# Kernel optimization log

Hardware: AMD Instinct MI355X
Metric: run time of the kernel (lower is better)

## Reference

```python
import jax, jax.numpy as jnp
import numpy as np
import math

B, S, D = 16, 256, 41
LATENT, NREF, NLAYERS, NHEADS = 128, 128, 3, 4


def setup_inputs() -> dict:
    key = jax.random.key(0)
    ks = jax.random.split(key, 12)
    time_x = jax.random.uniform(ks[0], (B, S), dtype=jnp.float32)
    value_x = jax.random.normal(ks[1], (B, S, D), dtype=jnp.float32)
    mask_x = jax.random.randint(ks[2], (B, S, D), 0, 2).astype(jnp.int32)
    s = 0.05
    Wi = jax.random.normal(ks[3], (D + 2, LATENT), dtype=jnp.float32) * s
    bi = jnp.zeros((LATENT,), jnp.float32)
    I = jax.random.normal(ks[4], (NLAYERS, NREF, LATENT), dtype=jnp.float32) * s
    # axis 1: 0 -> mab0 (induced->data), 1 -> mab1 (data->induced)
    Wq = jax.random.normal(ks[5], (NLAYERS, 2, LATENT, LATENT), dtype=jnp.float32) * s
    Wk = jax.random.normal(ks[6], (NLAYERS, 2, LATENT, LATENT), dtype=jnp.float32) * s
    Wv = jax.random.normal(ks[7], (NLAYERS, 2, LATENT, LATENT), dtype=jnp.float32) * s
    Wo = jax.random.normal(ks[8], (NLAYERS, 2, LATENT, LATENT), dtype=jnp.float32) * s
    bq = jnp.zeros((NLAYERS, 2, LATENT), jnp.float32)
    bk = jnp.zeros((NLAYERS, 2, LATENT), jnp.float32)
    bv = jnp.zeros((NLAYERS, 2, LATENT), jnp.float32)
    bo = jnp.zeros((NLAYERS, 2, LATENT), jnp.float32)
    return dict(time_x=time_x, value_x=value_x, mask_x=mask_x, Wi=Wi, bi=bi, I=I,
                Wq=Wq, bq=bq, Wk=Wk, bk=bk, Wv=Wv, bv=bv, Wo=Wo, bo=bo)


def _mab(Q, K, Wq, bq, Wk, bk, Wv, bv, Wo, bo, key_mask):
    # MAB2: multi-head attn (heads via split-last-dim), residual Q_, then O + relu(fc_o(O))
    dV = Wq.shape[1]
    dh = dV // NHEADS
    Bq, Lq, _ = Q.shape
    Qh = (Q @ Wq + bq).reshape(Bq, Lq, NHEADS, dh)
    Kh = (K @ Wk + bk).reshape(Bq, -1, NHEADS, dh)
    Vh = (K @ Wv + bv).reshape(Bq, -1, NHEADS, dh)
    att = jnp.einsum('bqhd,bkhd->bhqk', Qh, Kh) / math.sqrt(dV)
    if key_mask is not None:
        att = jnp.where(key_mask[:, None, None, :] == 0, -10e9, att)
    A = jax.nn.softmax(att, axis=-1)
    O = (Qh + jnp.einsum('bhqk,bkhd->bqhd', A, Vh)).reshape(Bq, Lq, dV)
    return O + jax.nn.relu(O @ Wo + bo)


def reference(time_x, value_x, mask_x, Wi, bi, I, Wq, bq, Wk, bk, Wv, bv, Wo, bo):
    L = S * D
    mflat = mask_x.reshape(B, L)
    # stable compaction: valid entries first, original row-major order preserved
    order = jnp.argsort(1 - mflat, axis=1)  # jnp.argsort is stable
    T = jnp.broadcast_to(time_x[:, :, None], (B, S, D)).reshape(B, L)
    C = jnp.broadcast_to(jnp.arange(D, dtype=jnp.int32), (B, S, D)).reshape(B, L)
    U = value_x.reshape(B, L)
    g = lambda a: jnp.take_along_axis(a, order, axis=1)
    T_, U_, C_, mk_i = g(T), g(U), g(C), g(mflat)
    mk = mk_i.astype(jnp.float32)  # [B, L]
    Coh = jax.nn.one_hot(C_, D, dtype=jnp.float32)
    X = jnp.concatenate([Coh, T_[..., None], U_[..., None]], axis=-1) * mk[..., None]
    Z = jax.nn.relu(X @ Wi + bi) * mk[..., None]  # Y_e, [B, L, LATENT]
    for l in range(NLAYERS):
        Ib = jnp.broadcast_to(I[l][None], (B, NREF, LATENT))
        H = _mab(Ib, Z, Wq[l, 0], bq[l, 0], Wk[l, 0], bk[l, 0], Wv[l, 0], bv[l, 0],
                 Wo[l, 0], bo[l, 0], mk)          # induced points attend to masked data
        O = _mab(Z, H, Wq[l, 1], bq[l, 1], Wk[l, 1], bk[l, 1], Wv[l, 1], bv[l, 1],
                 Wo[l, 1], bo[l, 1], None)        # data attends to induced points (all valid)
        Z = O * mk[..., None] + Z
    return Z, mk[..., None]
```

## Files before the change

### kernel.cpp

```cpp
#include <hip/hip_runtime.h>
#include <math.h>

#define BB 16
#define SS 256
#define DD 41
#define LL (SS*DD)
#define LAT 128
#define NH 4
#define NL 3
#define RSQ 0.08838834764831845f

typedef short bf16x8 __attribute__((ext_vector_type(8)));
typedef float f32x4 __attribute__((ext_vector_type(4)));
#define MFMA __builtin_amdgcn_mfma_f32_16x16x32_bf16

__device__ __forceinline__ unsigned short f2b(float f) {
    unsigned u = __builtin_bit_cast(unsigned, f);
    unsigned r = (u + 0x7FFFu + ((u >> 16) & 1u)) >> 16;
    return (unsigned short)r;
}
__device__ __forceinline__ float b2f(unsigned short h) {
    unsigned u = ((unsigned)h) << 16;
    return __builtin_bit_cast(float, u);
}

__global__ __launch_bounds__(256)
void k_compact(const float* __restrict__ time_x, const float* __restrict__ value_x,
               const int* __restrict__ mask_x,
               float* __restrict__ compT, float* __restrict__ compU,
               int* __restrict__ compC, int* __restrict__ nvalid)
{
    int b = blockIdx.x, tid = threadIdx.x;
    int lane = tid & 63, w = tid >> 6;
    __shared__ int sW[4];
    __shared__ int s_base;
    if (tid == 0) s_base = 0;
    __syncthreads();
    for (int j0 = 0; j0 < LL; j0 += 256) {
        int j = j0 + tid;
        int m = mask_x[b * LL + j];
        unsigned long long bal = __ballot(m != 0);
        int pre = __popcll(bal & ((1ull << lane) - 1ull));
        if (lane == 0) sW[w] = __popcll(bal);
        __syncthreads();
        int woff = 0;
        for (int i = 0; i < w; ++i) woff += sW[i];
        int tot = sW[0] + sW[1] + sW[2] + sW[3];
        if (m) {
            int pos = s_base + woff + pre;
            compT[b * LL + pos] = time_x[b * SS + j / DD];
            compU[b * LL + pos] = value_x[b * LL + j];
            compC[b * LL + pos] = j % DD;
        }
        __syncthreads();
        if (tid == 0) s_base += tot;
        __syncthreads();
    }
    if (tid == 0) nvalid[b] = s_base;
}

template<int UZ>
__global__ __launch_bounds__(256)
void k_init(const float* __restrict__ Wi, const float* __restrict__ bi,
            const float* __restrict__ compT, const float* __restrict__ compU,
            const int* __restrict__ compC, const int* __restrict__ nvalid,
            float* __restrict__ out, unsigned short* __restrict__ Zb)
{
    int b = blockIdx.y, p0 = blockIdx.x * 8, tid = threadIdx.x;
    float* Z = out;
    float* MK = out + (size_t)BB * LL * LAT;
    int nv = nvalid[b];
    for (int s = 0; s < 2; ++s) {
        int e = s * 256 + tid;
        int r = e >> 6, k2 = (e & 63) * 2;
        int p = p0 + r;
        size_t zi = ((size_t)b * LL + p) * LAT + k2;
        float v0 = 0.f, v1 = 0.f;
        if (p < nv) {
            int c = compC[b * LL + p];
            float t = compT[b * LL + p], u = compU[b * LL + p];
            v0 = fmaxf(Wi[c * LAT + k2]     + t * Wi[41 * LAT + k2]     + u * Wi[42 * LAT + k2]     + bi[k2],     0.f);
            v1 = fmaxf(Wi[c * LAT + k2 + 1] + t * Wi[41 * LAT + k2 + 1] + u * Wi[42 * LAT + k2 + 1] + bi[k2 + 1], 0.f);
        }
        *(float2*)&Z[zi] = make_float2(v0, v1);
        if constexpr (UZ) {
            unsigned short h2[2] = {f2b(v0), f2b(v1)};
            *(unsigned*)&Zb[((size_t)b * LL + p) * LAT + k2] = *(const unsigned*)h2;
        }
        if (k2 == 0) MK[b * LL + p] = (p < nv) ? 1.f : 0.f;
    }
}

__global__ __launch_bounds__(256)
void k_prep(const float* __restrict__ I, const float* __restrict__ Wq,
            const float* __restrict__ bq,
            const float* __restrict__ Wk, const float* __restrict__ Wv,
            const float* __restrict__ Wo,
            float* __restrict__ Qh0f, unsigned short* __restrict__ Qh0b,
            unsigned short* __restrict__ WkT, unsigned short* __restrict__ WvT,
            unsigned short* __restrict__ WqT, unsigned short* __restrict__ WoT)
{
    __shared__ float srow[128];
    int blk = blockIdx.x, tid = threadIdx.x, l = blockIdx.y;
    const float* Il  = I  + (size_t)l * 16384;
    const float* Wq0 = Wq + (size_t)(l * 2 + 0) * 16384;
    const float* bq0 = bq + (size_t)(l * 2 + 0) * 128;
    const float* Wk0 = Wk + (size_t)(l * 2 + 0) * 16384;
    const float* Wv0 = Wv + (size_t)(l * 2 + 0) * 16384;
    const float* Wq1 = Wq + (size_t)(l * 2 + 1) * 16384;
    const float* Wo1 = Wo + (size_t)(l * 2 + 1) * 16384;
    if (blk < 128) {
        if (tid < 128) srow[tid] = Il[blk * 128 + tid];
        __syncthreads();
        if (tid < 128) {
            float acc = bq0[tid];
            for (int i = 0; i < 128; ++i) acc += srow[i] * Wq0[i * 128 + tid];
            Qh0f[(size_t)l * 16384 + blk * 128 + tid] = acc;
            Qh0b[(size_t)l * 16384 + blk * 128 + tid] = f2b(acc);
        }
    } else {
        const float* src = (blk == 128) ? Wk0 : (blk == 129) ? Wv0 : (blk == 130) ? Wq1 : Wo1;
        unsigned short* dst = (blk == 128) ? WkT : (blk == 129) ? WvT : (blk == 130) ? WqT : WoT;
        dst += (size_t)l * 16384;
        for (int e = tid; e < 16384; e += 256) {
            int i = e >> 7, n = e & 127;
            dst[n * 128 + i] = f2b(src[e]);
        }
    }
}

template<int UZ>
__global__ __launch_bounds__(512, 4)
void k_flash0(const float* __restrict__ Z, const unsigned short* __restrict__ Zb,
              const unsigned short* __restrict__ Qh0b,
              const unsigned short* __restrict__ WkT, const unsigned short* __restrict__ WvT,
              const float* __restrict__ bk0, const float* __restrict__ bv0,
              const int* __restrict__ nvalid, float* __restrict__ ml,
              unsigned short* __restrict__ accp, int ks)
{
    const int chunk = blockIdx.x, b = blockIdx.y;
    const int tid = threadIdx.x, lane = tid & 63, w = tid >> 6;
    const int l16 = lane & 15, g4 = lane >> 4;
    const f32x4 fz = {0.f, 0.f, 0.f, 0.f};

    __shared__ unsigned short sZ[32 * 136];
    __shared__ unsigned short sKh[32 * 136];
    __shared__ unsigned short sVT[128 * 40];
    __shared__ float sS[128 * 33];
    __shared__ unsigned short sP[128 * 40];
    __shared__ float sM[NH * 128], sL[NH * 128], sScale[128];

    for (int e = tid; e < NH * 128; e += 512) { sM[e] = -1e30f; sL[e] = 0.f; }

    f32x4 acc[8];
    for (int n = 0; n < 8; ++n) acc[n] = fz;

    int nv = nvalid[b];
    int c0 = (int)(((long long)chunk * nv) / ks);
    int c1 = (int)(((long long)(chunk + 1) * nv) / ks);

    float bkd = bk0[w * 16 + l16];
    float bvd = bv0[w * 16 + l16];

    const int sr = tid >> 4, sc = (tid & 15) * 8;
    float4 pa, pb;
    uint4 pz;
    if (c0 < c1) {
        if constexpr (UZ) {
            pz = *(const uint4*)&Zb[((size_t)b * LL + c0 + sr) * LAT + sc];
        } else {
            const float* s = &Z[((size_t)b * LL + c0 + sr) * LAT + sc];
            pa = *(const float4*)s; pb = *(const float4*)(s + 4);
        }
    }

    __syncthreads();

    for (int kt = c0; kt < c1; kt += 32) {
        int nk = min(32, c1 - kt);
        if constexpr (UZ) {
            uint4 z4 = {0u, 0u, 0u, 0u};
            *(uint4*)&sZ[sr * 136 + sc] = (sr < nk) ? pz : z4;
        } else {
            bf16x8 v;
            if (sr < nk) {
                ((unsigned short*)&v)[0] = f2b(pa.x);
                ((unsigned short*)&v)[1] = f2b(pa.y);
                ((unsigned short*)&v)[2] = f2b(pa.z);
                ((unsigned short*)&v)[3] = f2b(pa.w);
                ((unsigned short*)&v)[4] = f2b(pb.x);
                ((unsigned short*)&v)[5] = f2b(pb.y);
                ((unsigned short*)&v)[6] = f2b(pb.z);
                ((unsigned short*)&v)[7] = f2b(pb.w);
            } else {
                #pragma unroll
                for (int j = 0; j < 8; ++j) ((unsigned short*)&v)[j] = 0;
            }
            *(bf16x8*)&sZ[sr * 136 + sc] = v;
        }
        __syncthreads();
        if (kt + 32 < c1) {
            if constexpr (UZ) {
                pz = *(const uint4*)&Zb[((size_t)b * LL + kt + 32 + sr) * LAT + sc];
            } else {
                const float* s = &Z[((size_t)b * LL + kt + 32 + sr) * LAT + sc];
                pa = *(const float4*)s; pb = *(const float4*)(s + 4);
            }
        }
        {
            f32x4 ck[2] = {fz, fz}, cv[2] = {fz, fz};
            #pragma unroll
            for (int k = 0; k < 4; ++k) {
                bf16x8 a0 = *(const bf16x8*)&sZ[(l16) * 136 + k * 32 + g4 * 8];
                bf16x8 a1 = *(const bf16x8*)&sZ[(16 + l16) * 136 + k * 32 + g4 * 8];
                bf16x8 bk_ = *(const bf16x8*)&WkT[(w * 16 + l16) * 128 + k * 32 + g4 * 8];
                bf16x8 bv_ = *(const bf16x8*)&WvT[(w * 16 + l16) * 128 + k * 32 + g4 * 8];
                ck[0] = MFMA(a0, bk_, ck[0], 0, 0, 0);
                ck[1] = MFMA(a1, bk_, ck[1], 0, 0, 0);
                cv[0] = MFMA(a0, bv_, cv[0], 0, 0, 0);
                cv[1] = MFMA(a1, bv_, cv[1], 0, 0, 0);
            }
            #pragma unroll
            for (int m = 0; m < 2; ++m)
                #pragma unroll
                for (int r = 0; r < 4; ++r) {
                    int kk = m * 16 + g4 * 4 + r;
                    int d = w * 16 + l16;
                    sKh[kk * 136 + d] = f2b(ck[m][r] + bkd);
                    sVT[d * 40 + kk] = f2b(cv[m][r] + bvd);
                }
        }
        __syncthreads();
        for (int h = 0; h < NH; ++h) {
            bf16x8 aq = *(const bf16x8*)&Qh0b[(w * 16 + l16) * 128 + h * 32 + g4 * 8];
            #pragma unroll
            for (int n = 0; n < 2; ++n) {
                bf16x8 bk_ = *(const bf16x8*)&sKh[(n * 16 + l16) * 136 + h * 32 + g4 * 8];
                f32x4 s = MFMA(aq, bk_, fz, 0, 0, 0);
                #pragma unroll
                for (int r = 0; r < 4; ++r)
                    sS[(w * 16 + g4 * 4 + r) * 33 + n * 16 + l16] = s[r] * RSQ;
            }
            int q = w * 16 + (lane >> 2);
            int k0 = (lane & 3) * 8;
            float sv[8];
            float mx = -1e30f;
            #pragma unroll
            for (int j = 0; j < 8; ++j) {
                int kk = k0 + j;
                sv[j] = (kk < nk) ? sS[q * 33 + kk] : -1e30f;
                mx = fmaxf(mx, sv[j]);
            }
            mx = fmaxf(mx, __shfl_xor(mx, 1));
            mx = fmaxf(mx, __shfl_xor(mx, 2));
            float mr = sM[h * 128 + q];
            float mn = fmaxf(mr, mx);
            float sc = __expf(mr - mn);
            float ls = 0.f;
            bf16x8 pv;
            #pragma unroll
            for (int j = 0; j < 8; ++j) {
                float p = (k0 + j < nk) ? __expf(sv[j] - mn) : 0.f;
                ((unsigned short*)&pv)[j] = f2b(p);
                ls += p;
            }
            *(bf16x8*)&sP[q * 40 + k0] = pv;
            ls += __shfl_xor(ls, 1);
            ls += __shfl_xor(ls, 2);
            if ((lane & 3) == 0) {
                sM[h * 128 + q] = mn;
                sL[h * 128 + q] = sL[h * 128 + q] * sc + ls;
                sScale[q] = sc;
            }
            #pragma unroll
            for (int nn = 0; nn < 2; ++nn) {
                int nt = 2 * h + nn;
                #pragma unroll
                for (int r = 0; r < 4; ++r) {
                    float scq = sScale[w * 16 + g4 * 4 + r];
                    acc[nt][r] *= scq;
                }
            }
            bf16x8 aP = *(const bf16x8*)&sP[(w * 16 + l16) * 40 + g4 * 8];
            #pragma unroll
            for (int nn = 0; nn < 2; ++nn) {
                bf16x8 bV = *(const bf16x8*)&sVT[(h * 32 + nn * 16 + l16) * 40 + g4 * 8];
                acc[2 * h + nn] = MFMA(aP, bV, acc[2 * h + nn], 0, 0, 0);
            }
        }
        __syncthreads();
    }
    __syncthreads();
    size_t mlbase = (((size_t)b * ks + chunk) * NH) * 128 * 2;
    for (int e = tid; e < NH * 128; e += 512) {
        ml[mlbase + e * 2 + 0] = sM[e];
        ml[mlbase + e * 2 + 1] = sL[e];
    }
    size_t abase = (((size_t)b * ks + chunk) * 128) * 128;
    #pragma unroll
    for (int n = 0; n < 8; ++n)
        #pragma unroll
        for (int r = 0; r < 4; ++r) {
            int q = w * 16 + g4 * 4 + r;
            int d = n * 16 + l16;
            accp[abase + (size_t)q * 128 + d] = f2b(acc[n][r]);
        }
}

__global__ __launch_bounds__(128)
void k_post0(const float* __restrict__ ml, const unsigned short* __restrict__ accp,
             const float* __restrict__ Qh0f,
             const float* __restrict__ Wo0, const float* __restrict__ bo0,
             const float* __restrict__ Wk1, const float* __restrict__ bk1,
             const float* __restrict__ Wv1, const float* __restrict__ bv1,
             unsigned short* __restrict__ Kh1b, unsigned short* __restrict__ Vh1Tb, int ks)
{
    int q = blockIdx.x, b = blockIdx.y, d = threadIdx.x, h = d >> 5;
    __shared__ float sx[128], sh2[128];
    float M = -1e30f;
    for (int c = 0; c < ks; ++c)
        M = fmaxf(M, ml[((((size_t)b * ks + c) * NH + h) * 128 + q) * 2]);
    float L = 0.f, A = 0.f;
    for (int c = 0; c < ks; ++c) {
        size_t base = ((((size_t)b * ks + c) * NH + h) * 128 + q) * 2;
        float sc = __expf(ml[base] - M);
        L += sc * ml[base + 1];
        A += sc * b2f(accp[(((size_t)b * ks + c) * 128 + q) * 128 + d]);
    }
    float o0 = Qh0f[q * 128 + d] + ((L > 0.f) ? A / L : 0.f);
    sx[d] = o0;
    __syncthreads();
    float acc = bo0[d];
    for (int i = 0; i < 128; ++i) acc += sx[i] * Wo0[i * 128 + d];
    float hv = o0 + fmaxf(acc, 0.f);
    sh2[d] = hv;
    __syncthreads();
    float ak = bk1[d], av = bv1[d];
    for (int i = 0; i < 128; ++i) {
        float x = sh2[i];
        ak += x * Wk1[i * 128 + d];
        av += x * Wv1[i * 128 + d];
    }
    Kh1b[((size_t)b * 128 + q) * 128 + d] = f2b(ak);
    Vh1Tb[((size_t)b * 128 + d) * 128 + q] = f2b(av);
}

template<int UZ>
__global__ __launch_bounds__(512, 6)
void k_mab1(float* __restrict__ Z, unsigned short* __restrict__ Zb,
            const unsigned short* __restrict__ Kh1b,
            const unsigned short* __restrict__ Vh1Tb,
            const unsigned short* __restrict__ WqT, const float* __restrict__ bq1,
            const unsigned short* __restrict__ WoT, const float* __restrict__ bo1,
            const int* __restrict__ nvalid, int writeZb)
{
    const int b = blockIdx.y;
    const int p0 = blockIdx.x * 64;
    const int nv = nvalid[b];
    if (p0 >= nv) return;
    const int tid = threadIdx.x, lane = tid & 63, w = tid >> 6;
    const int l16 = lane & 15, g4 = lane >> 4;
    const f32x4 fz = {0.f, 0.f, 0.f, 0.f};

    __shared__ unsigned short sQh[64 * 136];
    __shared__ unsigned short sU[8 * 16 * 136];
    float* sUf = (float*)sU;

    {
        int r = tid >> 3, c = (tid & 7) * 16;
        if constexpr (UZ) {
            const uint4* zsrc = (const uint4*)&Zb[((size_t)b * LL + p0 + r) * LAT + c];
            *(uint4*)&sU[r * 136 + c]     = zsrc[0];
            *(uint4*)&sU[r * 136 + c + 8] = zsrc[1];
        } else {
            const float* zr = &Z[((size_t)b * LL + p0 + r) * LAT + c];
            #pragma unroll
            for (int half = 0; half < 2; ++half) {
                float4 f0 = *(const float4*)(zr + half * 8);
                float4 f1 = *(const float4*)(zr + half * 8 + 4);
                bf16x8 v;
                ((unsigned short*)&v)[0] = f2b(f0.x);
                ((unsigned short*)&v)[1] = f2b(f0.y);
                ((unsigned short*)&v)[2] = f2b(f0.z);
                ((unsigned short*)&v)[3] = f2b(f0.w);
                ((unsigned short*)&v)[4] = f2b(f1.x);
                ((unsigned short*)&v)[5] = f2b(f1.y);
                ((unsigned short*)&v)[6] = f2b(f1.z);
                ((unsigned short*)&v)[7] = f2b(f1.w);
                *(bf16x8*)&sU[r * 136 + c + half * 8] = v;
            }
        }
    }
    __syncthreads();
    {
        f32x4 c4[4] = {fz, fz, fz, fz};
        #pragma unroll
        for (int ks = 0; ks < 4; ++ks) {
            bf16x8 bw = *(const bf16x8*)&WqT[(w * 16 + l16) * 128 + ks * 32 + g4 * 8];
            #pragma unroll
            for (int mt = 0; mt < 4; ++mt) {
                bf16x8 a = *(const bf16x8*)&sU[(mt * 16 + l16) * 136 + ks * 32 + g4 * 8];
                c4[mt] = MFMA(a, bw, c4[mt], 0, 0, 0);
            }
        }
        float bqv = bq1[w * 16 + l16];
        #pragma unroll
        for (int mt = 0; mt < 4; ++mt)
            #pragma unroll
            for (int r = 0; r < 4; ++r)
                sQh[(mt * 16 + g4 * 4 + r) * 136 + w * 16 + l16] = f2b(c4[mt][r] + bqv);
    }
    __syncthreads();

    const int t = w >> 1;
    const int hbase = (w & 1) * 2;
    unsigned short* ps = &sU[w * 16 * 136];
    f32x4 oacc[2][2];

    #pragma unroll
    for (int hh = 0; hh < 2; ++hh) {
        const int h = hbase + hh;
        f32x4 s[8];
        bf16x8 bq8 = *(const bf16x8*)&sQh[(t * 16 + l16) * 136 + h * 32 + g4 * 8];
        #pragma unroll
        for (int mt = 0; mt < 8; ++mt) {
            bf16x8 ak = *(const bf16x8*)&Kh1b[((size_t)b * 128 + mt * 16 + l16) * 128 + h * 32 + g4 * 8];
            s[mt] = MFMA(ak, bq8, fz, 0, 0, 0);
        }
        float mx = -1e30f;
        #pragma unroll
        for (int mt = 0; mt < 8; ++mt)
            #pragma unroll
            for (int r = 0; r < 4; ++r) mx = fmaxf(mx, s[mt][r]);
        mx = fmaxf(mx, __shfl_xor(mx, 16));
        mx = fmaxf(mx, __shfl_xor(mx, 32));
        float ls = 0.f;
        #pragma unroll
        for (int mt = 0; mt < 8; ++mt)
            #pragma unroll
            for (int r = 0; r < 4; ++r) {
                float p = __expf((s[mt][r] - mx) * RSQ);
                s[mt][r] = p;
                ls += p;
            }
        ls += __shfl_xor(ls, 16);
        ls += __shfl_xor(ls, 32);
        float inv = 1.f / ls;
        #pragma unroll
        for (int mt = 0; mt < 8; ++mt) {
            unsigned short p4[4];
            #pragma unroll
            for (int r = 0; r < 4; ++r) p4[r] = f2b(s[mt][r] * inv);
            *(uint2*)&ps[l16 * 136 + mt * 16 + g4 * 4] = *(const uint2*)p4;
        }
        #pragma unroll
        for (int nn = 0; nn < 2; ++nn) {
            f32x4 o = fz;
            #pragma unroll
            for (int ks = 0; ks < 4; ++ks) {
                bf16x8 aP = *(const bf16x8*)&ps[l16 * 136 + ks * 32 + g4 * 8];
                bf16x8 bV = *(const bf16x8*)&Vh1Tb[((size_t)b * 128 + h * 32 + nn * 16 + l16) * 128 + ks * 32 + g4 * 8];
                o = MFMA(aP, bV, o, 0, 0, 0);
            }
            oacc[hh][nn] = o;
        }
    }
    #pragma unroll
    for (int hh = 0; hh < 2; ++hh)
        #pragma unroll
        for (int nn = 0; nn < 2; ++nn) {
            int col = (hbase + hh) * 32 + nn * 16 + l16;
            #pragma unroll
            for (int r = 0; r < 4; ++r) {
                int row = t * 16 + g4 * 4 + r;
                float val = oacc[hh][nn][r] + b2f(sQh[row * 136 + col]);
                sQh[row * 136 + col] = f2b(val);
            }
        }
    __syncthreads();
    {
        f32x4 c4[4] = {fz, fz, fz, fz};
        #pragma unroll
        for (int ks = 0; ks < 4; ++ks) {
            bf16x8 bw = *(const bf16x8*)&WoT[(w * 16 + l16) * 128 + ks * 32 + g4 * 8];
            #pragma unroll
            for (int mt = 0; mt < 4; ++mt) {
                bf16x8 a = *(const bf16x8*)&sQh[(mt * 16 + l16) * 136 + ks * 32 + g4 * 8];
                c4[mt] = MFMA(a, bw, c4[mt], 0, 0, 0);
            }
        }
        float bov = bo1[w * 16 + l16];
        #pragma unroll
        for (int mt = 0; mt < 4; ++mt)
            #pragma unroll
            for (int r = 0; r < 4; ++r) {
                int row = mt * 16 + g4 * 4 + r;
                sUf[row * 132 + w * 16 + l16] = fmaxf(c4[mt][r] + bov, 0.f);
            }
    }
    __syncthreads();
    {
        int row = tid >> 3, cc = (tid & 7) * 16;
        if (p0 + row < nv) {
            size_t zi = ((size_t)b * LL + p0 + row) * LAT + cc;
            float vout[16];
            const unsigned short* ob = &sQh[row * 136 + cc];
            const float* rf = &sUf[row * 132 + cc];
            #pragma unroll
            for (int i = 0; i < 4; ++i) {
                float4 zv = *(const float4*)&Z[zi + i * 4];
                vout[i * 4 + 0] = zv.x + b2f(ob[i * 4 + 0]) + rf[i * 4 + 0];
                vout[i * 4 + 1] = zv.y + b2f(ob[i * 4 + 1]) + rf[i * 4 + 1];
                vout[i * 4 + 2] = zv.z + b2f(ob[i * 4 + 2]) + rf[i * 4 + 2];
                vout[i * 4 + 3] = zv.w + b2f(ob[i * 4 + 3]) + rf[i * 4 + 3];
            }
            #pragma unroll
            for (int i = 0; i < 4; ++i)
                *(float4*)&Z[zi + i * 4] = make_float4(vout[i*4], vout[i*4+1], vout[i*4+2], vout[i*4+3]);
            if constexpr (UZ) {
                if (writeZb) {
                    unsigned short hb[16];
                    #pragma unroll
                    for (int i = 0; i < 16; ++i) hb[i] = f2b(vout[i]);
                    *(uint4*)&Zb[((size_t)b * LL + p0 + row) * LAT + cc]     = *(const uint4*)&hb[0];
                    *(uint4*)&Zb[((size_t)b * LL + p0 + row) * LAT + cc + 8] = *(const uint4*)&hb[8];
                }
            }
        }
    }
}

extern "C" void kernel_launch(void* const* d_in, const int* in_sizes, int n_in,
                              void* d_out, int out_size, void* d_ws, size_t ws_size,
                              hipStream_t stream)
{
    const float* time_x  = (const float*)d_in[0];
    const float* value_x = (const float*)d_in[1];
    const int*   mask_x  = (const int*)d_in[2];
    const float* Wi = (const float*)d_in[3];
    const float* bi = (const float*)d_in[4];
    const float* I  = (const float*)d_in[5];
    const float* Wq = (const float*)d_in[6];
    const float* bq = (const float*)d_in[7];
    const float* Wk = (const float*)d_in[8];
    const float* bk = (const float*)d_in[9];
    const float* Wv = (const float*)d_in[10];
    const float* bv = (const float*)d_in[11];
    const float* Wo = (const float*)d_in[12];
    const float* bo = (const float*)d_in[13];
    float* out = (float*)d_out;

    const size_t BL = (size_t)BB * LL;
    const size_t base_fl = 3 * BL + 64 + (size_t)NL * 16384 + 5 * (size_t)NL * 8192
                         + 2 * (size_t)BB * 8192;
    const size_t ml_fl_32   = (size_t)BB * 32 * NH * 256;
    const size_t accp_fl_32 = (size_t)BB * 32 * 8192;
    const size_t zb_fl      = BL * 64 + 8192;
    const size_t need_big   = (base_fl + ml_fl_32 + accp_fl_32 + zb_fl) * 4;
    const int big = (ws_size >= need_big);
    const int ks = big ? 32 : 16;

    float* ws = (float*)d_ws;
    float* compT  = ws;                      ws += BL;
    float* compU  = ws;                      ws += BL;
    int*   compC  = (int*)ws;                ws += BL;
    int*   nvalid = (int*)ws;                ws += 64;
    float* Qh0f   = ws;                      ws += (size_t)NL * 16384;
    unsigned short* Qh0b  = (unsigned short*)ws;  ws += (size_t)NL * 8192;
    unsigned short* WkT   = (unsigned short*)ws;  ws += (size_t)NL * 8192;
    unsigned short* WvT   = (unsigned short*)ws;  ws += (size_t)NL * 8192;
    unsigned short* WqT   = (unsigned short*)ws;  ws += (size_t)NL * 8192;
    unsigned short* WoT   = (unsigned short*)ws;  ws += (size_t)NL * 8192;
    unsigned short* Kh1b  = (unsigned short*)ws;  ws += (size_t)BB * 8192;
    unsigned short* Vh1Tb = (unsigned short*)ws;  ws += (size_t)BB * 8192;
    float* ml     = ws;                      ws += (size_t)BB * ks * NH * 256;
    unsigned short* accp  = (unsigned short*)ws;  ws += (size_t)BB * ks * 8192;
    unsigned short* Zb    = (unsigned short*)ws;

    k_compact<<<BB, 256, 0, stream>>>(time_x, value_x, mask_x, compT, compU, compC, nvalid);
    if (big) k_init<1><<<dim3(LL / 8, BB), 256, 0, stream>>>(Wi, bi, compT, compU, compC, nvalid, out, Zb);
    else     k_init<0><<<dim3(LL / 8, BB), 256, 0, stream>>>(Wi, bi, compT, compU, compC, nvalid, out, Zb);
    k_prep<<<dim3(132, NL), 256, 0, stream>>>(I, Wq, bq, Wk, Wv, Wo,
                                              Qh0f, Qh0b, WkT, WvT, WqT, WoT);

    for (int l = 0; l < NL; ++l) {
        const float* Wo0 = Wo + (size_t)(l * 2 + 0) * 16384;
        const float* Wk1 = Wk + (size_t)(l * 2 + 1) * 16384;
        const float* Wv1 = Wv + (size_t)(l * 2 + 1) * 16384;
        const float* bk0 = bk + (l * 2 + 0) * 128;
        const float* bv0 = bv + (l * 2 + 0) * 128;
        const float* bo0 = bo + (l * 2 + 0) * 128;
        const float* bq1 = bq + (l * 2 + 1) * 128;
        const float* bk1 = bk + (l * 2 + 1) * 128;
        const float* bv1 = bv + (l * 2 + 1) * 128;
        const float* bo1 = bo + (l * 2 + 1) * 128;

        if (big)
            k_flash0<1><<<dim3(ks, BB), 512, 0, stream>>>(out, Zb, Qh0b + (size_t)l * 16384,
                                                          WkT + (size_t)l * 16384,
                                                          WvT + (size_t)l * 16384,
                                                          bk0, bv0, nvalid, ml, accp, ks);
        else
            k_flash0<0><<<dim3(ks, BB), 512, 0, stream>>>(out, Zb, Qh0b + (size_t)l * 16384,
                                                          WkT + (size_t)l * 16384,
                                                          WvT + (size_t)l * 16384,
                                                          bk0, bv0, nvalid, ml, accp, ks);
        k_post0<<<dim3(128, BB), 128, 0, stream>>>(ml, accp, Qh0f + (size_t)l * 16384,
                                                   Wo0, bo0, Wk1, bk1, Wv1, bv1, Kh1b, Vh1Tb, ks);
        int wzb = (l < NL - 1) ? 1 : 0;
        if (big)
            k_mab1<1><<<dim3(LL / 64, BB), 512, 0, stream>>>(out, Zb, Kh1b, Vh1Tb,
                                                             WqT + (size_t)l * 16384, bq1,
                                                             WoT + (size_t)l * 16384, bo1, nvalid, wzb);
        else
            k_mab1<0><<<dim3(LL / 64, BB), 512, 0, stream>>>(out, Zb, Kh1b, Vh1Tb,
                                                             WqT + (size_t)l * 16384, bq1,
                                                             WoT + (size_t)l * 16384, bo1, nvalid, wzb);
    }
}
```

Before: 574.0 us.

## Keep flash softmax state in registers, shrink mab1 tiles, raise key split

The flash kernel for the first attention block now computes transposed scores so each wave keeps its softmax max and sum in registers. This removes the shared score buffer, the shared row-stat arrays and the per-tile trailing barrier. The second-block kernel now works on 32-row tiles with 256 threads, one head per wave, and fuses the residual write directly from MFMA outputs, with no staging through shared memory. The key-split count can also rise to 64 when workspace allows, which adds parallelism at the cost of more partial results to merge and less coalesced final Z stores.

```diff
diff --git a/kernel.cpp b/kernel.cpp
--- a/kernel.cpp
+++ b/kernel.cpp
@@ -146,14 +146,14 @@
     __shared__ unsigned short sZ[32 * 136];
     __shared__ unsigned short sKh[32 * 136];
     __shared__ unsigned short sVT[128 * 40];
-    __shared__ float sS[128 * 33];
-    __shared__ unsigned short sP[128 * 40];
-    __shared__ float sM[NH * 128], sL[NH * 128], sScale[128];
-
-    for (int e = tid; e < NH * 128; e += 512) { sM[e] = -1e30f; sL[e] = 0.f; }
+    __shared__ unsigned short sPw[8][16 * 40];
 
     f32x4 acc[8];
+    #pragma unroll
     for (int n = 0; n < 8; ++n) acc[n] = fz;
+    float mreg[NH], lreg[NH];
+    #pragma unroll
+    for (int h = 0; h < NH; ++h) { mreg[h] = -1e30f; lreg[h] = 0.f; }
 
     int nv = nvalid[b];
     int c0 = (int)(((long long)chunk * nv) / ks);
@@ -161,6 +161,7 @@
 
     float bkd = bk0[w * 16 + l16];
     float bvd = bv0[w * 16 + l16];
+    unsigned short* ps = sPw[w];
 
     const int sr = tid >> 4, sc = (tid & 15) * 8;
     float4 pa, pb;
@@ -173,8 +174,6 @@
             pa = *(const float4*)s; pb = *(const float4*)(s + 4);
         }
     }
-
-    __syncthreads();
 
     for (int kt = c0; kt < c1; kt += 32) {
         int nk = min(32, c1 - kt);
@@ -231,72 +230,69 @@
                 }
         }
         __syncthreads();
+        #pragma unroll
         for (int h = 0; h < NH; ++h) {
-            bf16x8 aq = *(const bf16x8*)&Qh0b[(w * 16 + l16) * 128 + h * 32 + g4 * 8];
-            #pragma unroll
-            for (int n = 0; n < 2; ++n) {
-                bf16x8 bk_ = *(const bf16x8*)&sKh[(n * 16 + l16) * 136 + h * 32 + g4 * 8];
-                f32x4 s = MFMA(aq, bk_, fz, 0, 0, 0);
-                #pragma unroll
-                for (int r = 0; r < 4; ++r)
-                    sS[(w * 16 + g4 * 4 + r) * 33 + n * 16 + l16] = s[r] * RSQ;
-            }
-            int q = w * 16 + (lane >> 2);
-            int k0 = (lane & 3) * 8;
-            float sv[8];
+            bf16x8 bq = *(const bf16x8*)&Qh0b[(w * 16 + l16) * 128 + h * 32 + g4 * 8];
+            f32x4 s0 = MFMA(*(const bf16x8*)&sKh[(l16) * 136 + h * 32 + g4 * 8], bq, fz, 0, 0, 0);
+            f32x4 s1 = MFMA(*(const bf16x8*)&sKh[(16 + l16) * 136 + h * 32 + g4 * 8], bq, fz, 0, 0, 0);
+            float sv[2][4];
             float mx = -1e30f;
             #pragma unroll
-            for (int j = 0; j < 8; ++j) {
-                int kk = k0 + j;
-                sv[j] = (kk < nk) ? sS[q * 33 + kk] : -1e30f;
-                mx = fmaxf(mx, sv[j]);
-            }
-            mx = fmaxf(mx, __shfl_xor(mx, 1));
-            mx = fmaxf(mx, __shfl_xor(mx, 2));
-            float mr = sM[h * 128 + q];
-            float mn = fmaxf(mr, mx);
-            float sc = __expf(mr - mn);
-            float ls = 0.f;
-            bf16x8 pv;
-            #pragma unroll
-            for (int j = 0; j < 8; ++j) {
-                float p = (k0 + j < nk) ? __expf(sv[j] - mn) : 0.f;
-                ((unsigned short*)&pv)[j] = f2b(p);
-                ls += p;
-            }
-            *(bf16x8*)&sP[q * 40 + k0] = pv;
-            ls += __shfl_xor(ls, 1);
-            ls += __shfl_xor(ls, 2);
-            if ((lane & 3) == 0) {
-                sM[h * 128 + q] = mn;
-                sL[h * 128 + q] = sL[h * 128 + q] * sc + ls;
-                sScale[q] = sc;
-            }
-            #pragma unroll
-            for (int nn = 0; nn < 2; ++nn) {
-                int nt = 2 * h + nn;
+            for (int mt = 0; mt < 2; ++mt)
                 #pragma unroll
                 for (int r = 0; r < 4; ++r) {
-                    float scq = sScale[w * 16 + g4 * 4 + r];
-                    acc[nt][r] *= scq;
+                    int key = mt * 16 + g4 * 4 + r;
+                    float v = (key < nk) ? ((mt ? s1[r] : s0[r]) * RSQ) : -1e30f;
+                    sv[mt][r] = v;
+                    mx = fmaxf(mx, v);
                 }
-            }
-            bf16x8 aP = *(const bf16x8*)&sP[(w * 16 + l16) * 40 + g4 * 8];
+            mx = fmaxf(mx, __shfl_xor(mx, 16));
+            mx = fmaxf(mx, __shfl_xor(mx, 32));
+            float mo = mreg[h];
+            float mn = fmaxf(mo, mx);
+            float scl = __expf(mo - mn);
+            float ls = 0.f;
+            unsigned short p4[2][4];
+            #pragma unroll
+            for (int mt = 0; mt < 2; ++mt)
+                #pragma unroll
+                for (int r = 0; r < 4; ++r) {
+                    int key = mt * 16 + g4 * 4 + r;
+                    float p = (key < nk) ? __expf(sv[mt][r] - mn) : 0.f;
+                    p4[mt][r] = f2b(p);
+                    ls += p;
+                }
+            ls += __shfl_xor(ls, 16);
+            ls += __shfl_xor(ls, 32);
+            mreg[h] = mn;
+            lreg[h] = lreg[h] * scl + ls;
+            *(uint2*)&ps[l16 * 40 + g4 * 4]      = *(const uint2*)p4[0];
+            *(uint2*)&ps[l16 * 40 + 16 + g4 * 4] = *(const uint2*)p4[1];
+            float scq[4];
+            #pragma unroll
+            for (int r = 0; r < 4; ++r) scq[r] = __shfl(scl, g4 * 4 + r);
+            #pragma unroll
+            for (int nn = 0; nn < 2; ++nn)
+                #pragma unroll
+                for (int r = 0; r < 4; ++r) acc[2 * h + nn][r] *= scq[r];
+            bf16x8 aP = *(const bf16x8*)&ps[l16 * 40 + g4 * 8];
             #pragma unroll
             for (int nn = 0; nn < 2; ++nn) {
                 bf16x8 bV = *(const bf16x8*)&sVT[(h * 32 + nn * 16 + l16) * 40 + g4 * 8];
                 acc[2 * h + nn] = MFMA(aP, bV, acc[2 * h + nn], 0, 0, 0);
             }
         }
-        __syncthreads();
-    }
-    __syncthreads();
-    size_t mlbase = (((size_t)b * ks + chunk) * NH) * 128 * 2;
-    for (int e = tid; e < NH * 128; e += 512) {
-        ml[mlbase + e * 2 + 0] = sM[e];
-        ml[mlbase + e * 2 + 1] = sL[e];
-    }
-    size_t abase = (((size_t)b * ks + chunk) * 128) * 128;
+    }
+    size_t mlbase = ((size_t)((size_t)b * ks + chunk) * NH) * 128 * 2;
+    if (g4 == 0) {
+        int q = w * 16 + l16;
+        #pragma unroll
+        for (int h = 0; h < NH; ++h) {
+            ml[mlbase + ((size_t)h * 128 + q) * 2 + 0] = mreg[h];
+            ml[mlbase + ((size_t)h * 128 + q) * 2 + 1] = lreg[h];
+        }
+    }
+    size_t abase = ((size_t)((size_t)b * ks + chunk) * 128) * 128;
     #pragma unroll
     for (int n = 0; n < 8; ++n)
         #pragma unroll
@@ -346,7 +342,7 @@
 }
 
 template<int UZ>
-__global__ __launch_bounds__(512, 6)
+__global__ __launch_bounds__(256, 5)
 void k_mab1(float* __restrict__ Z, unsigned short* __restrict__ Zb,
             const unsigned short* __restrict__ Kh1b,
             const unsigned short* __restrict__ Vh1Tb,
@@ -355,16 +351,15 @@
             const int* __restrict__ nvalid, int writeZb)
 {
     const int b = blockIdx.y;
-    const int p0 = blockIdx.x * 64;
+    const int p0 = blockIdx.x * 32;
     const int nv = nvalid[b];
     if (p0 >= nv) return;
     const int tid = threadIdx.x, lane = tid & 63, w = tid >> 6;
     const int l16 = lane & 15, g4 = lane >> 4;
     const f32x4 fz = {0.f, 0.f, 0.f, 0.f};
 
-    __shared__ unsigned short sQh[64 * 136];
-    __shared__ unsigned short sU[8 * 16 * 136];
-    float* sUf = (float*)sU;
+    __shared__ unsigned short sQh[32 * 136];
+    __shared__ unsigned short sU[4 * 16 * 136];
 
     {
         int r = tid >> 3, c = (tid & 7) * 16;
@@ -392,36 +387,36 @@
         }
     }
     __syncthreads();
-    {
-        f32x4 c4[4] = {fz, fz, fz, fz};
-        #pragma unroll
-        for (int ks = 0; ks < 4; ++ks) {
-            bf16x8 bw = *(const bf16x8*)&WqT[(w * 16 + l16) * 128 + ks * 32 + g4 * 8];
-            #pragma unroll
-            for (int mt = 0; mt < 4; ++mt) {
-                bf16x8 a = *(const bf16x8*)&sU[(mt * 16 + l16) * 136 + ks * 32 + g4 * 8];
-                c4[mt] = MFMA(a, bw, c4[mt], 0, 0, 0);
-            }
-        }
-        float bqv = bq1[w * 16 + l16];
-        #pragma unroll
-        for (int mt = 0; mt < 4; ++mt)
+    #pragma unroll
+    for (int ct = 0; ct < 2; ++ct) {
+        f32x4 c2[2] = {fz, fz};
+        int col = w * 32 + ct * 16 + l16;
+        #pragma unroll
+        for (int ks4 = 0; ks4 < 4; ++ks4) {
+            bf16x8 bw = *(const bf16x8*)&WqT[col * 128 + ks4 * 32 + g4 * 8];
+            #pragma unroll
+            for (int mt = 0; mt < 2; ++mt) {
+                bf16x8 a = *(const bf16x8*)&sU[(mt * 16 + l16) * 136 + ks4 * 32 + g4 * 8];
+                c2[mt] = MFMA(a, bw, c2[mt], 0, 0, 0);
+            }
+        }
+        float bqv = bq1[col];
+        #pragma unroll
+        for (int mt = 0; mt < 2; ++mt)
             #pragma unroll
             for (int r = 0; r < 4; ++r)
-                sQh[(mt * 16 + g4 * 4 + r) * 136 + w * 16 + l16] = f2b(c4[mt][r] + bqv);
+                sQh[(mt * 16 + g4 * 4 + r) * 136 + col] = f2b(c2[mt][r] + bqv);
     }
     __syncthreads();
 
-    const int t = w >> 1;
-    const int hbase = (w & 1) * 2;
     unsigned short* ps = &sU[w * 16 * 136];
+    const int h = w;
     f32x4 oacc[2][2];
 
     #pragma unroll
-    for (int hh = 0; hh < 2; ++hh) {
-        const int h = hbase + hh;
+    for (int qt = 0; qt < 2; ++qt) {
+        bf16x8 bq8 = *(const bf16x8*)&sQh[(qt * 16 + l16) * 136 + h * 32 + g4 * 8];
         f32x4 s[8];
-        bf16x8 bq8 = *(const bf16x8*)&sQh[(t * 16 + l16) * 136 + h * 32 + g4 * 8];
         #pragma unroll
         for (int mt = 0; mt < 8; ++mt) {
             bf16x8 ak = *(const bf16x8*)&Kh1b[((size_t)b * 128 + mt * 16 + l16) * 128 + h * 32 + g4 * 8];
@@ -457,76 +452,55 @@
         for (int nn = 0; nn < 2; ++nn) {
             f32x4 o = fz;
             #pragma unroll
-            for (int ks = 0; ks < 4; ++ks) {
-                bf16x8 aP = *(const bf16x8*)&ps[l16 * 136 + ks * 32 + g4 * 8];
-                bf16x8 bV = *(const bf16x8*)&Vh1Tb[((size_t)b * 128 + h * 32 + nn * 16 + l16) * 128 + ks * 32 + g4 * 8];
+            for (int ks4 = 0; ks4 < 4; ++ks4) {
+                bf16x8 aP = *(const bf16x8*)&ps[l16 * 136 + ks4 * 32 + g4 * 8];
+                bf16x8 bV = *(const bf16x8*)&Vh1Tb[((size_t)b * 128 + h * 32 + nn * 16 + l16) * 128 + ks4 * 32 + g4 * 8];
                 o = MFMA(aP, bV, o, 0, 0, 0);
             }
-            oacc[hh][nn] = o;
-        }
-    }
-    #pragma unroll
-    for (int hh = 0; hh < 2; ++hh)
+            oacc[qt][nn] = o;
+        }
+    }
+    #pragma unroll
+    for (int qt = 0; qt < 2; ++qt)
         #pragma unroll
         for (int nn = 0; nn < 2; ++nn) {
-            int col = (hbase + hh) * 32 + nn * 16 + l16;
+            int col = h * 32 + nn * 16 + l16;
             #pragma unroll
             for (int r = 0; r < 4; ++r) {
-                int row = t * 16 + g4 * 4 + r;
-                float val = oacc[hh][nn][r] + b2f(sQh[row * 136 + col]);
+                int row = qt * 16 + g4 * 4 + r;
+                float val = oacc[qt][nn][r] + b2f(sQh[row * 136 + col]);
                 sQh[row * 136 + col] = f2b(val);
             }
         }
     __syncthreads();
-    {
-        f32x4 c4[4] = {fz, fz, fz, fz};
-        #pragma unroll
-        for (int ks = 0; ks < 4; ++ks) {
-            bf16x8 bw = *(const bf16x8*)&WoT[(w * 16 + l16) * 128 + ks * 32 + g4 * 8];
-            #pragma unroll
-            for (int mt = 0; mt < 4; ++mt) {
-                bf16x8 a = *(const bf16x8*)&sQh[(mt * 16 + l16) * 136 + ks * 32 + g4 * 8];
-                c4[mt] = MFMA(a, bw, c4[mt], 0, 0, 0);
-            }
-        }
-        float bov = bo1[w * 16 + l16];
-        #pragma unroll
-        for (int mt = 0; mt < 4; ++mt)
+    #pragma unroll
+    for (int ct = 0; ct < 2; ++ct) {
+        f32x4 c2[2] = {fz, fz};
+        int col = w * 32 + ct * 16 + l16;
+        #pragma unroll
+        for (int ks4 = 0; ks4 < 4; ++ks4) {
+            bf16x8 bw = *(const bf16x8*)&WoT[col * 128 + ks4 * 32 + g4 * 8];
+            #pragma unroll
+            for (int mt = 0; mt < 2; ++mt) {
+                bf16x8 a = *(const bf16x8*)&sQh[(mt * 16 + l16) * 136 + ks4 * 32 + g4 * 8];
+                c2[mt] = MFMA(a, bw, c2[mt], 0, 0, 0);
+            }
+        }
+        float bov = bo1[col];
+        #pragma unroll
+        for (int mt = 0; mt < 2; ++mt)
             #pragma unroll
             for (int r = 0; r < 4; ++r) {
                 int row = mt * 16 + g4 * 4 + r;
-                sUf[row * 132 + w * 16 + l16] = fmaxf(c4[mt][r] + bov, 0.f);
-            }
-    }
-    __syncthreads();
-    {
-        int row = tid >> 3, cc = (tid & 7) * 16;
-        if (p0 + row < nv) {
-            size_t zi = ((size_t)b * LL + p0 + row) * LAT + cc;
-            float vout[16];
-            const unsigned short* ob = &sQh[row * 136 + cc];
-            const float* rf = &sUf[row * 132 + cc];
-            #pragma unroll
-            for (int i = 0; i < 4; ++i) {
-                float4 zv = *(const float4*)&Z[zi + i * 4];
-                vout[i * 4 + 0] = zv.x + b2f(ob[i * 4 + 0]) + rf[i * 4 + 0];
-                vout[i * 4 + 1] = zv.y + b2f(ob[i * 4 + 1]) + rf[i * 4 + 1];
-                vout[i * 4 + 2] = zv.z + b2f(ob[i * 4 + 2]) + rf[i * 4 + 2];
-                vout[i * 4 + 3] = zv.w + b2f(ob[i * 4 + 3]) + rf[i * 4 + 3];
-            }
-            #pragma unroll
-            for (int i = 0; i < 4; ++i)
-                *(float4*)&Z[zi + i * 4] = make_float4(vout[i*4], vout[i*4+1], vout[i*4+2], vout[i*4+3]);
-            if constexpr (UZ) {
-                if (writeZb) {
-                    unsigned short hb[16];
-                    #pragma unroll
-                    for (int i = 0; i < 16; ++i) hb[i] = f2b(vout[i]);
-                    *(uint4*)&Zb[((size_t)b * LL + p0 + row) * LAT + cc]     = *(const uint4*)&hb[0];
-                    *(uint4*)&Zb[((size_t)b * LL + p0 + row) * LAT + cc + 8] = *(const uint4*)&hb[8];
+                if (p0 + row < nv) {
+                    size_t zi = ((size_t)b * LL + p0 + row) * LAT + col;
+                    float val = Z[zi] + b2f(sQh[row * 136 + col]) + fmaxf(c2[mt][r] + bov, 0.f);
+                    Z[zi] = val;
+                    if constexpr (UZ) {
+                        if (writeZb) Zb[((size_t)b * LL + p0 + row) * LAT + col] = f2b(val);
+                    }
                 }
             }
-        }
     }
 }
 
@@ -553,12 +527,15 @@
     const size_t BL = (size_t)BB * LL;
     const size_t base_fl = 3 * BL + 64 + (size_t)NL * 16384 + 5 * (size_t)NL * 8192
                          + 2 * (size_t)BB * 8192;
-    const size_t ml_fl_32   = (size_t)BB * 32 * NH * 256;
-    const size_t accp_fl_32 = (size_t)BB * 32 * 8192;
-    const size_t zb_fl      = BL * 64 + 8192;
-    const size_t need_big   = (base_fl + ml_fl_32 + accp_fl_32 + zb_fl) * 4;
-    const int big = (ws_size >= need_big);
-    const int ks = big ? 32 : 16;
+    const size_t zb_fl = BL * 64 + 8192;
+    auto need = [&](int kss) -> size_t {
+        size_t fl = base_fl + (size_t)BB * kss * NH * 256 + (size_t)BB * kss * 8192 + zb_fl;
+        return fl * 4;
+    };
+    int big, ks;
+    if (ws_size >= need(64))      { big = 1; ks = 64; }
+    else if (ws_size >= need(32)) { big = 1; ks = 32; }
+    else                          { big = 0; ks = 16; }
 
     float* ws = (float*)d_ws;
     float* compT  = ws;                      ws += BL;
@@ -609,11 +586,11 @@
                                                    Wo0, bo0, Wk1, bk1, Wv1, bv1, Kh1b, Vh1Tb, ks);
         int wzb = (l < NL - 1) ? 1 : 0;
         if (big)
-            k_mab1<1><<<dim3(LL / 64, BB), 512, 0, stream>>>(out, Zb, Kh1b, Vh1Tb,
+            k_mab1<1><<<dim3(LL / 32, BB), 256, 0, stream>>>(out, Zb, Kh1b, Vh1Tb,
                                                              WqT + (size_t)l * 16384, bq1,
                                                              WoT + (size_t)l * 16384, bo1, nvalid, wzb);
         else
-            k_mab1<0><<<dim3(LL / 64, BB), 512, 0, stream>>>(out, Zb, Kh1b, Vh1Tb,
+            k_mab1<0><<<dim3(LL / 32, BB), 256, 0, stream>>>(out, Zb, Kh1b, Vh1Tb,
                                                              WqT + (size_t)l * 16384, bq1,
                                                              WoT + (size_t)l * 16384, bo1, nvalid, wzb);
     }
```

New measurement: 645.5 us. 12.5% more time.
